# Kernel optimization log

Measured on AMD Instinct MI355X. Metric: run time of the kernel, lower is better.

## Reference

```python
import jax, jax.numpy as jnp
import numpy as np

EMB_DIM = 384
HEAD = 6
HEAD_DIM = EMB_DIM // HEAD  # 64


def setup_inputs() -> dict:
    key = jax.random.key(0)
    ks = jax.random.split(key, 6)
    B, N, D = 8, 2048, EMB_DIM
    s = 1.0 / np.sqrt(D)
    return {
        "z": jax.random.normal(ks[0], (B, N, D), dtype=jnp.float32),
        "w_q": jax.random.normal(ks[1], (D, D), dtype=jnp.float32) * s,
        "w_k": jax.random.normal(ks[2], (D, D), dtype=jnp.float32) * s,
        "w_v": jax.random.normal(ks[3], (D, D), dtype=jnp.float32) * s,
        "w_o": jax.random.normal(ks[4], (D, D), dtype=jnp.float32) * s,
        "b_o": jax.random.normal(ks[5], (D,), dtype=jnp.float32) * 0.02,
    }


def reference(z, w_q, w_k, w_v, w_o, b_o):
    B, N, D = z.shape
    H, Hd = HEAD, HEAD_DIM
    # QKV projections (bias-free Linear: x @ W^T)
    q = (z @ w_q.T).reshape(B, N, H, Hd).transpose(0, 2, 1, 3)  # (B,H,N,Hd)
    k = (z @ w_k.T).reshape(B, N, H, Hd).transpose(0, 2, 1, 3)
    v = (z @ w_v.T).reshape(B, N, H, Hd).transpose(0, 2, 1, 3)
    scores = jnp.einsum("bhqd,bhkd->bhqk", q, k) / np.sqrt(Hd)  # (B,H,N,N)
    attn = jax.nn.softmax(scores, axis=-1)
    out = jnp.einsum("bhqk,bhkd->bhqd", attn, v)  # (B,H,N,Hd)
    out = out.transpose(0, 2, 1, 3).reshape(B, N, D)
    return out @ w_o.T + b_o
```

## Files before the change

### kernel.cpp

```cpp
#include <hip/hip_runtime.h>


#define BN 8
#define NN 2048
#define DD 384
#define HH 6
#define MM (BN * NN)

typedef __attribute__((ext_vector_type(8))) short short8;
typedef __attribute__((ext_vector_type(4))) short sh4;
typedef __attribute__((ext_vector_type(4))) float f32x4;

#define MFMA_B16(a, b, c) __builtin_amdgcn_mfma_f32_16x16x32_bf16(a, b, c, 0, 0, 0)

__device__ __forceinline__ unsigned short f2b(float x) {
  unsigned int u = __builtin_bit_cast(unsigned int, x);
  u += 0x7fffu + ((u >> 16) & 1u);
  return (unsigned short)(u >> 16);
}

__device__ __forceinline__ short8 cvt8(float4 a, float4 b) {
  short8 r;
  r[0] = (short)f2b(a.x); r[1] = (short)f2b(a.y);
  r[2] = (short)f2b(a.z); r[3] = (short)f2b(a.w);
  r[4] = (short)f2b(b.x); r[5] = (short)f2b(b.y);
  r[6] = (short)f2b(b.z); r[7] = (short)f2b(b.w);
  return r;
}

__device__ __forceinline__ int swz128(int row, int byteInRow) {
  return row * 128 + (byteInRow ^ ((row & 7) << 4));
}

__global__ __launch_bounds__(256) void qkv_proj(
    const float* __restrict__ z, const float* __restrict__ wq,
    const float* __restrict__ wk, const float* __restrict__ wv,
    unsigned short* __restrict__ Qb, unsigned short* __restrict__ Kb,
    unsigned short* __restrict__ Vb) {
  __shared__ __align__(16) unsigned char smem[128 * 128 + 64 * 128];
  unsigned char* AsB = smem;
  unsigned char* BsB = smem + 128 * 128;

  const int t = threadIdx.x;
  const int m0 = blockIdx.x * 128;
  const int ct = blockIdx.y;
  const int proj = ct / 6;
  const int h = ct % 6;
  const int jcol = h * 64;
  const float* W = (proj == 0) ? wq : (proj == 1) ? wk : wv;
  const float oscale = (proj == 0) ? 0.125f : 1.0f;

  const int w = t >> 6;
  const int lane = t & 63;
  const int l15 = lane & 15;
  const int l4 = lane >> 4;

  f32x4 acc[2][4] = {};

  for (int k0 = 0; k0 < DD; k0 += 64) {
    __syncthreads();
#pragma unroll
    for (int l = 0; l < 4; ++l) {
      int idx = l * 256 + t;
      int row = idx >> 3, e = idx & 7;
      const float* p = &z[(size_t)(m0 + row) * DD + k0 + e * 8];
      float4 a = *(const float4*)p;
      float4 b = *(const float4*)(p + 4);
      *(short8*)(AsB + swz128(row, e * 16)) = cvt8(a, b);
    }
#pragma unroll
    for (int l = 0; l < 2; ++l) {
      int idx = l * 256 + t;
      int row = idx >> 3, e = idx & 7;
      const float* p = &W[(size_t)(jcol + row) * DD + k0 + e * 8];
      float4 a = *(const float4*)p;
      float4 b = *(const float4*)(p + 4);
      *(short8*)(BsB + swz128(row, e * 16)) = cvt8(a, b);
    }
    __syncthreads();

#pragma unroll
    for (int kc = 0; kc < 2; ++kc) {
      short8 af[2], bf[4];
#pragma unroll
      for (int fr = 0; fr < 2; ++fr)
        af[fr] = *(const short8*)(AsB +
                 swz128(w * 32 + fr * 16 + l15, kc * 64 + l4 * 16));
#pragma unroll
      for (int cb = 0; cb < 4; ++cb)
        bf[cb] = *(const short8*)(BsB +
                 swz128(cb * 16 + l15, kc * 64 + l4 * 16));
#pragma unroll
      for (int fr = 0; fr < 2; ++fr)
#pragma unroll
        for (int cb = 0; cb < 4; ++cb)
          acc[fr][cb] = MFMA_B16(af[fr], bf[cb], acc[fr][cb]);
    }
  }

  const int bb0 = m0 >> 11;
  if (proj != 2) {
    unsigned short* Ob = (proj == 0) ? Qb : Kb;
#pragma unroll
    for (int fr = 0; fr < 2; ++fr)
#pragma unroll
      for (int r = 0; r < 4; ++r) {
        int m = m0 + w * 32 + fr * 16 + l4 * 4 + r;
        int n = m & (NN - 1);
        unsigned short* dst = &Ob[(((size_t)(bb0 * HH + h)) * NN + n) * 64];
#pragma unroll
        for (int cb = 0; cb < 4; ++cb)
          dst[cb * 16 + l15] = f2b(acc[fr][cb][r] * oscale);
      }
  } else {
    __syncthreads();
    unsigned short* T = (unsigned short*)smem;
#pragma unroll
    for (int fr = 0; fr < 2; ++fr)
#pragma unroll
      for (int r = 0; r < 4; ++r) {
        int ml = w * 32 + fr * 16 + l4 * 4 + r;
#pragma unroll
        for (int cb = 0; cb < 4; ++cb)
          T[(cb * 16 + l15) * 136 + ml] = f2b(acc[fr][cb][r]);
      }
    __syncthreads();
    const int n0 = m0 & (NN - 1);
#pragma unroll
    for (int l = 0; l < 4; ++l) {
      int idx = l * 256 + t;
      int row = idx >> 4, col = (idx & 15) * 8;
      short8 v = *(const short8*)&T[row * 136 + col];
      *(short8*)&Vb[(((size_t)(bb0 * HH + h)) * 64 + row) * NN + n0 + col] = v;
    }
  }
}

__global__ __launch_bounds__(256) void flash_attn(
    const unsigned short* __restrict__ Qb, const unsigned short* __restrict__ Kb,
    const unsigned short* __restrict__ Vtb, unsigned short* __restrict__ Ab) {
  __shared__ __align__(16) unsigned char KsB[64 * 128];
  __shared__ __align__(16) unsigned char VsB[64 * 128];
  __shared__ __align__(16) unsigned short PsS[64 * 72];

  const int t = threadIdx.x;
  const int qt = blockIdx.x;
  const int bh = blockIdx.y;
  const int w = t >> 6;
  const int lane = t & 63;
  const int l15 = lane & 15;
  const int l4 = lane >> 4;

  const unsigned short* Kbase = Kb + (size_t)bh * NN * 64;
  const unsigned short* Vtbase = Vtb + (size_t)bh * 64 * NN;

  short8 q[2];
  {
    const unsigned short* Qp =
        Qb + ((size_t)bh * NN + qt * 64 + w * 16 + l15) * 64;
    q[0] = *(const short8*)&Qp[l4 * 8];
    q[1] = *(const short8*)&Qp[32 + l4 * 8];
  }

  f32x4 o[4] = {};
  float mreg = -1e30f, lreg = 0.f;

  const int krow = t >> 2, khalf = t & 3;

  for (int kt = 0; kt < NN / 64; ++kt) {
    __syncthreads();
    {
      const unsigned short* Kp =
          Kbase + ((size_t)(kt * 64 + krow)) * 64 + khalf * 16;
      short8 a = *(const short8*)&Kp[0];
      short8 b = *(const short8*)&Kp[8];
      *(short8*)(KsB + swz128(krow, khalf * 32)) = a;
      *(short8*)(KsB + swz128(krow, khalf * 32 + 16)) = b;
      const unsigned short* Vp =
          Vtbase + (size_t)krow * NN + kt * 64 + khalf * 16;
      short8 c = *(const short8*)&Vp[0];
      short8 d = *(const short8*)&Vp[8];
      *(short8*)(VsB + swz128(krow, khalf * 32)) = c;
      *(short8*)(VsB + swz128(krow, khalf * 32 + 16)) = d;
    }
    __syncthreads();

    f32x4 sacc[4] = {};
#pragma unroll
    for (int kc = 0; kc < 2; ++kc) {
      short8 kf[4];
#pragma unroll
      for (int cb = 0; cb < 4; ++cb)
        kf[cb] =
            *(const short8*)(KsB + swz128(cb * 16 + l15, kc * 64 + l4 * 16));
#pragma unroll
      for (int cb = 0; cb < 4; ++cb)
        sacc[cb] = MFMA_B16(kf[cb], q[kc], sacc[cb]);
    }

    float tm = -1e30f;
#pragma unroll
    for (int cb = 0; cb < 4; ++cb)
#pragma unroll
      for (int r = 0; r < 4; ++r) tm = fmaxf(tm, sacc[cb][r]);
    tm = fmaxf(tm, __shfl_xor(tm, 16, 64));
    tm = fmaxf(tm, __shfl_xor(tm, 32, 64));
    float mnew = fmaxf(mreg, tm);
    float sc = __expf(mreg - mnew);
    float ps = 0.f;
#pragma unroll
    for (int cb = 0; cb < 4; ++cb)
#pragma unroll
      for (int r = 0; r < 4; ++r) {
        float p = __expf(sacc[cb][r] - mnew);
        sacc[cb][r] = p;
        ps += p;
      }
    ps += __shfl_xor(ps, 16, 64);
    ps += __shfl_xor(ps, 32, 64);
    lreg = lreg * sc + ps;
    mreg = mnew;
#pragma unroll
    for (int db = 0; db < 4; ++db) o[db] *= sc;

#pragma unroll
    for (int cb = 0; cb < 4; ++cb) {
      sh4 pv;
#pragma unroll
      for (int r = 0; r < 4; ++r) pv[r] = (short)f2b(sacc[cb][r]);
      *(sh4*)&PsS[(w * 16 + l15) * 72 + cb * 16 + l4 * 4] = pv;
    }

#pragma unroll
    for (int kc = 0; kc < 2; ++kc) {
      short8 pf =
          *(const short8*)&PsS[(w * 16 + l15) * 72 + kc * 32 + l4 * 8];
      short8 vf[4];
#pragma unroll
      for (int db = 0; db < 4; ++db)
        vf[db] =
            *(const short8*)(VsB + swz128(db * 16 + l15, kc * 64 + l4 * 16));
#pragma unroll
      for (int db = 0; db < 4; ++db)
        o[db] = MFMA_B16(vf[db], pf, o[db]);
    }
  }

  const int bb = bh / HH, h = bh % HH;
  const float inv = 1.f / lreg;
  const int n = qt * 64 + w * 16 + l15;
  unsigned short* dst = &Ab[((size_t)(bb * NN + n)) * DD + h * 64];
#pragma unroll
  for (int db = 0; db < 4; ++db) {
    sh4 ov;
#pragma unroll
    for (int r = 0; r < 4; ++r) ov[r] = (short)f2b(o[db][r] * inv);
    *(sh4*)&dst[db * 16 + l4 * 4] = ov;
  }
}

__global__ __launch_bounds__(256) void out_proj(
    const unsigned short* __restrict__ Ab, const float* __restrict__ wo,
    const float* __restrict__ bo, float* __restrict__ out) {
  __shared__ __align__(16) unsigned char AsB[128 * 128];
  __shared__ __align__(16) unsigned char BsB[64 * 128];

  const int t = threadIdx.x;
  const int m0 = blockIdx.x * 128;
  const int jcol = blockIdx.y * 64;
  const int w = t >> 6;
  const int lane = t & 63;
  const int l15 = lane & 15;
  const int l4 = lane >> 4;

  f32x4 acc[2][4] = {};

  for (int k0 = 0; k0 < DD; k0 += 64) {
    __syncthreads();
#pragma unroll
    for (int l = 0; l < 4; ++l) {
      int idx = l * 256 + t;
      int row = idx >> 3, e = idx & 7;
      short8 v = *(const short8*)&Ab[(size_t)(m0 + row) * DD + k0 + e * 8];
      *(short8*)(AsB + swz128(row, e * 16)) = v;
    }
#pragma unroll
    for (int l = 0; l < 2; ++l) {
      int idx = l * 256 + t;
      int row = idx >> 3, e = idx & 7;
      const float* p = &wo[(size_t)(jcol + row) * DD + k0 + e * 8];
      float4 a = *(const float4*)p;
      float4 b = *(const float4*)(p + 4);
      *(short8*)(BsB + swz128(row, e * 16)) = cvt8(a, b);
    }
    __syncthreads();

#pragma unroll
    for (int kc = 0; kc < 2; ++kc) {
      short8 af[2], bf[4];
#pragma unroll
      for (int fr = 0; fr < 2; ++fr)
        af[fr] = *(const short8*)(AsB +
                 swz128(w * 32 + fr * 16 + l15, kc * 64 + l4 * 16));
#pragma unroll
      for (int cb = 0; cb < 4; ++cb)
        bf[cb] = *(const short8*)(BsB +
                 swz128(cb * 16 + l15, kc * 64 + l4 * 16));
#pragma unroll
      for (int fr = 0; fr < 2; ++fr)
#pragma unroll
        for (int cb = 0; cb < 4; ++cb)
          acc[fr][cb] = MFMA_B16(af[fr], bf[cb], acc[fr][cb]);
    }
  }

#pragma unroll
  for (int fr = 0; fr < 2; ++fr)
#pragma unroll
    for (int r = 0; r < 4; ++r) {
      int m = m0 + w * 32 + fr * 16 + l4 * 4 + r;
      float* dst = &out[(size_t)m * DD + jcol];
#pragma unroll
      for (int cb = 0; cb < 4; ++cb) {
        int c = cb * 16 + l15;
        dst[c] = acc[fr][cb][r] + bo[jcol + c];
      }
    }
}

extern "C" void kernel_launch(void* const* d_in, const int* in_sizes, int n_in,
                              void* d_out, int out_size, void* d_ws,
                              size_t ws_size, hipStream_t stream) {
  const float* z = (const float*)d_in[0];
  const float* wq = (const float*)d_in[1];
  const float* wk = (const float*)d_in[2];
  const float* wv = (const float*)d_in[3];
  const float* wo = (const float*)d_in[4];
  const float* bo = (const float*)d_in[5];
  float* out = (float*)d_out;

  const size_t plane = (size_t)MM * DD;
  unsigned short* Qb = (unsigned short*)d_ws;
  unsigned short* Kb = Qb + plane;
  unsigned short* Vb = Kb + plane;
  unsigned short* Ab = Vb + plane;

  qkv_proj<<<dim3(MM / 128, 18), 256, 0, stream>>>(z, wq, wk, wv, Qb, Kb, Vb);
  flash_attn<<<dim3(NN / 64, BN * HH), 256, 0, stream>>>(Qb, Kb, Vb, Ab);
  out_proj<<<dim3(MM / 128, DD / 64), 256, 0, stream>>>(Ab, wo, bo, out);
}
```

Baseline: 247.9 us.

## Pre-convert inputs to bf16, enlarge GEMM tiles, lazy-rescale exp2 softmax

A new prep kernel converts z and all four weight matrices to bf16 once, so the GEMMs stop re-converting fp32 tiles on every load. The QKV and output projection GEMMs move from 128x64 to 128x128 tiles with a 2x2 wave layout, which raises operand reuse per LDS load. Flash attention now uses exp2 with log2(e) folded into the Q scale, and only rescales the running max when it grows by more than 8. It also packs bf16 with v_cvt_pk_bf16_f32. The costs are an extra launch plus a full fp32-to-bf16 read/write pass over z, and larger register accumulators per thread.

New measurement: 223.4 us. 9.9% less time.

```diff
diff --git a/kernel.cpp b/kernel.cpp
--- a/kernel.cpp
+++ b/kernel.cpp
@@ -6,9 +6,10 @@
 #define DD 384
 #define HH 6
 #define MM (BN * NN)
+#define ZN (MM * DD)
+#define WN (DD * DD)
 
 typedef __attribute__((ext_vector_type(8))) short short8;
-typedef __attribute__((ext_vector_type(4))) short sh4;
 typedef __attribute__((ext_vector_type(4))) float f32x4;
 
 #define MFMA_B16(a, b, c) __builtin_amdgcn_mfma_f32_16x16x32_bf16(a, b, c, 0, 0, 0)
@@ -28,34 +29,65 @@
   return r;
 }
 
+__device__ __forceinline__ unsigned int cvtpk(float lo, float hi) {
+  unsigned int r;
+  asm("v_cvt_pk_bf16_f32 %0, %1, %2" : "=v"(r) : "v"(lo), "v"(hi));
+  return r;
+}
+
+__device__ __forceinline__ float exp2_(float x) {
+#if __has_builtin(__builtin_amdgcn_exp2f)
+  return __builtin_amdgcn_exp2f(x);
+#else
+  return exp2f(x);
+#endif
+}
+
 __device__ __forceinline__ int swz128(int row, int byteInRow) {
   return row * 128 + (byteInRow ^ ((row & 7) << 4));
 }
 
-__global__ __launch_bounds__(256) void qkv_proj(
+__global__ __launch_bounds__(256) void prep_bf16(
     const float* __restrict__ z, const float* __restrict__ wq,
     const float* __restrict__ wk, const float* __restrict__ wv,
+    const float* __restrict__ wo, unsigned short* __restrict__ zb,
+    unsigned short* __restrict__ wb) {
+  int i = (blockIdx.x * 256 + threadIdx.x) * 8;
+  const float* s;
+  unsigned short* d;
+  if (i < ZN) { s = z + i; d = zb + i; }
+  else if (i < ZN + WN) { s = wq + (i - ZN); d = wb + (i - ZN); }
+  else if (i < ZN + 2 * WN) { s = wk + (i - ZN - WN); d = wb + (i - ZN); }
+  else if (i < ZN + 3 * WN) { s = wv + (i - ZN - 2 * WN); d = wb + (i - ZN); }
+  else { s = wo + (i - ZN - 3 * WN); d = wb + (i - ZN); }
+  float4 a = *(const float4*)s;
+  float4 b = *(const float4*)(s + 4);
+  *(short8*)d = cvt8(a, b);
+}
+
+__global__ __launch_bounds__(256) void qkv_gemm(
+    const unsigned short* __restrict__ zb, const unsigned short* __restrict__ wb,
     unsigned short* __restrict__ Qb, unsigned short* __restrict__ Kb,
     unsigned short* __restrict__ Vb) {
-  __shared__ __align__(16) unsigned char smem[128 * 128 + 64 * 128];
+  __shared__ __align__(16) unsigned char smem[128 * 136 * 2];
   unsigned char* AsB = smem;
   unsigned char* BsB = smem + 128 * 128;
 
   const int t = threadIdx.x;
   const int m0 = blockIdx.x * 128;
-  const int ct = blockIdx.y;
-  const int proj = ct / 6;
-  const int h = ct % 6;
-  const int jcol = h * 64;
-  const float* W = (proj == 0) ? wq : (proj == 1) ? wk : wv;
-  const float oscale = (proj == 0) ? 0.125f : 1.0f;
+  const int cb9 = blockIdx.y;
+  const int proj = cb9 / 3;
+  const int jc = (cb9 % 3) * 128;
+  const int h0 = (cb9 % 3) * 2;
+  const unsigned short* Wp = wb + (size_t)proj * WN;
 
   const int w = t >> 6;
+  const int wr = w >> 1, wc = w & 1;
   const int lane = t & 63;
   const int l15 = lane & 15;
   const int l4 = lane >> 4;
 
-  f32x4 acc[2][4] = {};
+  f32x4 acc[4][4] = {};
 
   for (int k0 = 0; k0 < DD; k0 += 64) {
     __syncthreads();
@@ -63,35 +95,31 @@
     for (int l = 0; l < 4; ++l) {
       int idx = l * 256 + t;
       int row = idx >> 3, e = idx & 7;
-      const float* p = &z[(size_t)(m0 + row) * DD + k0 + e * 8];
-      float4 a = *(const float4*)p;
-      float4 b = *(const float4*)(p + 4);
-      *(short8*)(AsB + swz128(row, e * 16)) = cvt8(a, b);
-    }
-#pragma unroll
-    for (int l = 0; l < 2; ++l) {
+      short8 v = *(const short8*)&zb[(size_t)(m0 + row) * DD + k0 + e * 8];
+      *(short8*)(AsB + swz128(row, e * 16)) = v;
+    }
+#pragma unroll
+    for (int l = 0; l < 4; ++l) {
       int idx = l * 256 + t;
       int row = idx >> 3, e = idx & 7;
-      const float* p = &W[(size_t)(jcol + row) * DD + k0 + e * 8];
-      float4 a = *(const float4*)p;
-      float4 b = *(const float4*)(p + 4);
-      *(short8*)(BsB + swz128(row, e * 16)) = cvt8(a, b);
+      short8 v = *(const short8*)&Wp[(size_t)(jc + row) * DD + k0 + e * 8];
+      *(short8*)(BsB + swz128(row, e * 16)) = v;
     }
     __syncthreads();
 
 #pragma unroll
     for (int kc = 0; kc < 2; ++kc) {
-      short8 af[2], bf[4];
-#pragma unroll
-      for (int fr = 0; fr < 2; ++fr)
+      short8 af[4], bf[4];
+#pragma unroll
+      for (int fr = 0; fr < 4; ++fr)
         af[fr] = *(const short8*)(AsB +
-                 swz128(w * 32 + fr * 16 + l15, kc * 64 + l4 * 16));
+                 swz128(wr * 64 + fr * 16 + l15, kc * 64 + l4 * 16));
 #pragma unroll
       for (int cb = 0; cb < 4; ++cb)
         bf[cb] = *(const short8*)(BsB +
-                 swz128(cb * 16 + l15, kc * 64 + l4 * 16));
-#pragma unroll
-      for (int fr = 0; fr < 2; ++fr)
+                 swz128(wc * 64 + cb * 16 + l15, kc * 64 + l4 * 16));
+#pragma unroll
+      for (int fr = 0; fr < 4; ++fr)
 #pragma unroll
         for (int cb = 0; cb < 4; ++cb)
           acc[fr][cb] = MFMA_B16(af[fr], bf[cb], acc[fr][cb]);
@@ -99,39 +127,43 @@
   }
 
   const int bb0 = m0 >> 11;
-  if (proj != 2) {
+  const int n0 = m0 & (NN - 1);
+  if (proj < 2) {
+    const float osc = (proj == 0) ? 0.18033688011112042f : 1.0f;
     unsigned short* Ob = (proj == 0) ? Qb : Kb;
 #pragma unroll
-    for (int fr = 0; fr < 2; ++fr)
+    for (int fr = 0; fr < 4; ++fr)
 #pragma unroll
       for (int r = 0; r < 4; ++r) {
-        int m = m0 + w * 32 + fr * 16 + l4 * 4 + r;
-        int n = m & (NN - 1);
-        unsigned short* dst = &Ob[(((size_t)(bb0 * HH + h)) * NN + n) * 64];
-#pragma unroll
-        for (int cb = 0; cb < 4; ++cb)
-          dst[cb * 16 + l15] = f2b(acc[fr][cb][r] * oscale);
+        int n = n0 + wr * 64 + fr * 16 + l4 * 4 + r;
+#pragma unroll
+        for (int cb = 0; cb < 4; ++cb) {
+          int c = wc * 64 + cb * 16 + l15;
+          int h = h0 + (c >> 6), d = c & 63;
+          Ob[(((size_t)(bb0 * HH + h)) * NN + n) * 64 + d] =
+              f2b(acc[fr][cb][r] * osc);
+        }
       }
   } else {
     __syncthreads();
     unsigned short* T = (unsigned short*)smem;
 #pragma unroll
-    for (int fr = 0; fr < 2; ++fr)
+    for (int fr = 0; fr < 4; ++fr)
 #pragma unroll
       for (int r = 0; r < 4; ++r) {
-        int ml = w * 32 + fr * 16 + l4 * 4 + r;
+        int ml = wr * 64 + fr * 16 + l4 * 4 + r;
 #pragma unroll
         for (int cb = 0; cb < 4; ++cb)
-          T[(cb * 16 + l15) * 136 + ml] = f2b(acc[fr][cb][r]);
+          T[(wc * 64 + cb * 16 + l15) * 136 + ml] = f2b(acc[fr][cb][r]);
       }
     __syncthreads();
-    const int n0 = m0 & (NN - 1);
-#pragma unroll
-    for (int l = 0; l < 4; ++l) {
-      int idx = l * 256 + t;
-      int row = idx >> 4, col = (idx & 15) * 8;
-      short8 v = *(const short8*)&T[row * 136 + col];
-      *(short8*)&Vb[(((size_t)(bb0 * HH + h)) * 64 + row) * NN + n0 + col] = v;
+#pragma unroll
+    for (int l = 0; l < 8; ++l) {
+      int idx = l * 256 + t;
+      int cr = idx >> 4, nc = (idx & 15) * 8;
+      int h = h0 + (cr >> 6), d = cr & 63;
+      short8 v = *(const short8*)&T[cr * 136 + nc];
+      *(short8*)&Vb[(((size_t)(bb0 * HH + h)) * 64 + d) * NN + n0 + nc] = v;
     }
   }
 }
@@ -205,30 +237,33 @@
       for (int r = 0; r < 4; ++r) tm = fmaxf(tm, sacc[cb][r]);
     tm = fmaxf(tm, __shfl_xor(tm, 16, 64));
     tm = fmaxf(tm, __shfl_xor(tm, 32, 64));
-    float mnew = fmaxf(mreg, tm);
-    float sc = __expf(mreg - mnew);
+    if (__any(tm > mreg + 8.f)) {
+      float mnew = fmaxf(mreg, tm);
+      float sc = exp2_(mreg - mnew);
+#pragma unroll
+      for (int db = 0; db < 4; ++db) o[db] *= sc;
+      lreg *= sc;
+      mreg = mnew;
+    }
     float ps = 0.f;
 #pragma unroll
     for (int cb = 0; cb < 4; ++cb)
 #pragma unroll
       for (int r = 0; r < 4; ++r) {
-        float p = __expf(sacc[cb][r] - mnew);
+        float p = exp2_(sacc[cb][r] - mreg);
         sacc[cb][r] = p;
         ps += p;
       }
     ps += __shfl_xor(ps, 16, 64);
     ps += __shfl_xor(ps, 32, 64);
-    lreg = lreg * sc + ps;
-    mreg = mnew;
-#pragma unroll
-    for (int db = 0; db < 4; ++db) o[db] *= sc;
+    lreg += ps;
 
 #pragma unroll
     for (int cb = 0; cb < 4; ++cb) {
-      sh4 pv;
-#pragma unroll
-      for (int r = 0; r < 4; ++r) pv[r] = (short)f2b(sacc[cb][r]);
-      *(sh4*)&PsS[(w * 16 + l15) * 72 + cb * 16 + l4 * 4] = pv;
+      uint2 pw;
+      pw.x = cvtpk(sacc[cb][0], sacc[cb][1]);
+      pw.y = cvtpk(sacc[cb][2], sacc[cb][3]);
+      *(uint2*)&PsS[(w * 16 + l15) * 72 + cb * 16 + l4 * 4] = pw;
     }
 
 #pragma unroll
@@ -252,28 +287,30 @@
   unsigned short* dst = &Ab[((size_t)(bb * NN + n)) * DD + h * 64];
 #pragma unroll
   for (int db = 0; db < 4; ++db) {
-    sh4 ov;
-#pragma unroll
-    for (int r = 0; r < 4; ++r) ov[r] = (short)f2b(o[db][r] * inv);
-    *(sh4*)&dst[db * 16 + l4 * 4] = ov;
+    uint2 ov;
+    ov.x = cvtpk(o[db][0] * inv, o[db][1] * inv);
+    ov.y = cvtpk(o[db][2] * inv, o[db][3] * inv);
+    *(uint2*)&dst[db * 16 + l4 * 4] = ov;
   }
 }
 
 __global__ __launch_bounds__(256) void out_proj(
-    const unsigned short* __restrict__ Ab, const float* __restrict__ wo,
+    const unsigned short* __restrict__ Ab, const unsigned short* __restrict__ wob,
     const float* __restrict__ bo, float* __restrict__ out) {
-  __shared__ __align__(16) unsigned char AsB[128 * 128];
-  __shared__ __align__(16) unsigned char BsB[64 * 128];
+  __shared__ __align__(16) unsigned char smem[2 * 128 * 128];
+  unsigned char* AsB = smem;
+  unsigned char* BsB = smem + 128 * 128;
 
   const int t = threadIdx.x;
   const int m0 = blockIdx.x * 128;
-  const int jcol = blockIdx.y * 64;
+  const int jc = blockIdx.y * 128;
   const int w = t >> 6;
+  const int wr = w >> 1, wc = w & 1;
   const int lane = t & 63;
   const int l15 = lane & 15;
   const int l4 = lane >> 4;
 
-  f32x4 acc[2][4] = {};
+  f32x4 acc[4][4] = {};
 
   for (int k0 = 0; k0 < DD; k0 += 64) {
     __syncthreads();
@@ -285,29 +322,27 @@
       *(short8*)(AsB + swz128(row, e * 16)) = v;
     }
 #pragma unroll
-    for (int l = 0; l < 2; ++l) {
+    for (int l = 0; l < 4; ++l) {
       int idx = l * 256 + t;
       int row = idx >> 3, e = idx & 7;
-      const float* p = &wo[(size_t)(jcol + row) * DD + k0 + e * 8];
-      float4 a = *(const float4*)p;
-      float4 b = *(const float4*)(p + 4);
-      *(short8*)(BsB + swz128(row, e * 16)) = cvt8(a, b);
+      short8 v = *(const short8*)&wob[(size_t)(jc + row) * DD + k0 + e * 8];
+      *(short8*)(BsB + swz128(row, e * 16)) = v;
     }
     __syncthreads();
 
 #pragma unroll
     for (int kc = 0; kc < 2; ++kc) {
-      short8 af[2], bf[4];
-#pragma unroll
-      for (int fr = 0; fr < 2; ++fr)
+      short8 af[4], bf[4];
+#pragma unroll
+      for (int fr = 0; fr < 4; ++fr)
         af[fr] = *(const short8*)(AsB +
-                 swz128(w * 32 + fr * 16 + l15, kc * 64 + l4 * 16));
+                 swz128(wr * 64 + fr * 16 + l15, kc * 64 + l4 * 16));
 #pragma unroll
       for (int cb = 0; cb < 4; ++cb)
         bf[cb] = *(const short8*)(BsB +
-                 swz128(cb * 16 + l15, kc * 64 + l4 * 16));
-#pragma unroll
-      for (int fr = 0; fr < 2; ++fr)
+                 swz128(wc * 64 + cb * 16 + l15, kc * 64 + l4 * 16));
+#pragma unroll
+      for (int fr = 0; fr < 4; ++fr)
 #pragma unroll
         for (int cb = 0; cb < 4; ++cb)
           acc[fr][cb] = MFMA_B16(af[fr], bf[cb], acc[fr][cb]);
@@ -315,15 +350,15 @@
   }
 
 #pragma unroll
-  for (int fr = 0; fr < 2; ++fr)
+  for (int fr = 0; fr < 4; ++fr)
 #pragma unroll
     for (int r = 0; r < 4; ++r) {
-      int m = m0 + w * 32 + fr * 16 + l4 * 4 + r;
-      float* dst = &out[(size_t)m * DD + jcol];
+      int m = m0 + wr * 64 + fr * 16 + l4 * 4 + r;
+      float* dst = &out[(size_t)m * DD + jc];
 #pragma unroll
       for (int cb = 0; cb < 4; ++cb) {
-        int c = cb * 16 + l15;
-        dst[c] = acc[fr][cb][r] + bo[jcol + c];
+        int c = wc * 64 + cb * 16 + l15;
+        dst[c] = acc[fr][cb][r] + bo[jc + c];
       }
     }
 }
@@ -339,13 +374,18 @@
   const float* bo = (const float*)d_in[5];
   float* out = (float*)d_out;
 
-  const size_t plane = (size_t)MM * DD;
-  unsigned short* Qb = (unsigned short*)d_ws;
+  const size_t plane = (size_t)ZN;
+  unsigned short* zb = (unsigned short*)d_ws;
+  unsigned short* Qb = zb + plane;
   unsigned short* Kb = Qb + plane;
   unsigned short* Vb = Kb + plane;
-  unsigned short* Ab = Vb + plane;
-
-  qkv_proj<<<dim3(MM / 128, 18), 256, 0, stream>>>(z, wq, wk, wv, Qb, Kb, Vb);
+  unsigned short* wb = Vb + plane;
+  unsigned short* wob = wb + 3 * (size_t)WN;
+  unsigned short* Ab = zb;
+
+  prep_bf16<<<dim3((ZN + 4 * WN) / 2048), 256, 0, stream>>>(z, wq, wk, wv, wo,
+                                                            zb, wb);
+  qkv_gemm<<<dim3(MM / 128, 9), 256, 0, stream>>>(zb, wb, Qb, Kb, Vb);
   flash_attn<<<dim3(NN / 64, BN * HH), 256, 0, stream>>>(Qb, Kb, Vb, Ab);
-  out_proj<<<dim3(MM / 128, DD / 64), 256, 0, stream>>>(Ab, wo, bo, out);
-}
+  out_proj<<<dim3(MM / 128, DD / 128), 256, 0, stream>>>(Ab, wob, bo, out);
+}
```
